# Kernel optimization log

Hardware: AMD Instinct MI355X
Metric: run time of the kernel (lower is better)

The kernel has to match this reference:

```python
import jax, jax.numpy as jnp
import numpy as np

B, T, LD, PD, W, NL = 2048, 256, 32, 8, 64, 3
TH, CH = LD * 2, W * 2  # token/channel mixing hidden dims (expansion=2)


def setup_inputs() -> dict:
    key = jax.random.key(0)
    ks = jax.random.split(key, 12)
    n = lambda k, s, sc=0.02: jax.random.normal(k, s, jnp.float32) * sc
    return {
        "phys": jax.random.normal(ks[0], (B, T, PD), jnp.float32),
        "latents": jax.random.uniform(ks[1], (B, LD), jnp.float32),
        "pos_emb": n(ks[2], (1, LD, W)),
        "tokW": n(ks[3], (1, W)), "tokb": jnp.zeros((W,), jnp.float32),
        "physW1": n(ks[4], (PD, W)), "physb1": jnp.zeros((W,), jnp.float32),
        "physW2": n(ks[5], (W, W)), "physb2": jnp.zeros((W,), jnp.float32),
        "tn_g": jnp.ones((NL, W), jnp.float32), "tn_b": jnp.zeros((NL, W), jnp.float32),
        "tiW": n(ks[6], (NL, LD, TH)), "tib": jnp.zeros((NL, TH), jnp.float32),
        "toW": n(ks[7], (NL, TH, LD)), "tob": jnp.zeros((NL, LD), jnp.float32),
        "cn_g": jnp.ones((NL, W), jnp.float32), "cn_b": jnp.zeros((NL, W), jnp.float32),
        "ciW": n(ks[8], (NL, W, CH)), "cib": jnp.zeros((NL, CH), jnp.float32),
        "coW": n(ks[9], (NL, CH, W)), "cob": jnp.zeros((NL, W), jnp.float32),
        "hn_g": jnp.ones((W,), jnp.float32), "hn_b": jnp.zeros((W,), jnp.float32),
        "headW": n(ks[10], (W, 1), 0.0002),  # 0.02 init * 0.01 scaling from torch
        "headb": jnp.zeros((1,), jnp.float32),
    }


def _ln(x, g, b):
    m = jnp.mean(x, -1, keepdims=True)
    v = jnp.mean((x - m) ** 2, -1, keepdims=True)
    return (x - m) * jax.lax.rsqrt(v + 1e-5) * g + b


def reference(phys, latents, pos_emb, tokW, tokb, physW1, physb1, physW2, physb2,
              tn_g, tn_b, tiW, tib, toW, tob, cn_g, cn_b, ciW, cib, coW, cob,
              hn_g, hn_b, headW, headb):
    gelu = lambda x: jax.nn.gelu(x, approximate=False)  # torch nn.GELU default (exact)

    def step(current, phys_t):
        # token_projection of current[..., None]: Linear(1, W)
        tokens = current[:, :, None] * tokW[0] + tokb  # [B, LD, W]
        p = gelu(phys_t @ physW1 + physb1) @ physW2 + physb2  # [B, W]
        tokens = tokens + p[:, None, :] + pos_emb
        for i in range(NL):
            # token mixing: LN over width, mix across latent tokens
            mt = jnp.swapaxes(_ln(tokens, tn_g[i], tn_b[i]), 1, 2)  # [B, W, LD]
            mt = gelu(mt @ tiW[i] + tib[i]) @ toW[i] + tob[i]       # [B, W, LD]
            tokens = tokens + jnp.swapaxes(mt, 1, 2)
            # channel mixing over width
            mc = _ln(tokens, cn_g[i], cn_b[i])
            tokens = tokens + (gelu(mc @ ciW[i] + cib[i]) @ coW[i] + cob[i])
        delta = (_ln(tokens, hn_g, hn_b) @ headW + headb)[..., 0]  # [B, LD]
        new = jnp.clip(current + delta, 0.0, 1.0)
        return new, new

    _, outs = jax.lax.scan(step, latents, jnp.swapaxes(phys, 0, 1))  # [T, B, LD]
    return jnp.swapaxes(outs, 0, 1)  # [B, T, LD]
```

## Files before the change

### kernel.cpp

```cpp
#include <hip/hip_runtime.h>
#include <math.h>


namespace {
constexpr int Tt = 256, NL = 3;

typedef float    f32x4 __attribute__((ext_vector_type(4)));
typedef _Float16 half2 __attribute__((ext_vector_type(2)));
typedef _Float16 h16x8 __attribute__((ext_vector_type(8)));

#define MFMA16(a, b, c) __builtin_amdgcn_mfma_f32_16x16x32_f16((a), (b), (c), 0, 0, 0)

__device__ __forceinline__ half2 h2c(float v) { return (half2)((_Float16)v); }
__device__ __forceinline__ half2 pkrtz(float a, float b) {
    return __builtin_bit_cast(half2, __builtin_amdgcn_cvt_pkrtz(a, b));
}
__device__ __forceinline__ void st4h(short* p, half2 a, half2 b) {
    uint2 v;
    v.x = __builtin_bit_cast(unsigned int, a);
    v.y = __builtin_bit_cast(unsigned int, b);
    *(uint2*)p = v;
}
__device__ __forceinline__ half2 gelu_pk(half2 x) {
    half2 tc = __builtin_elementwise_min(__builtin_elementwise_max(x, h2c(-3.0f)), h2c(3.0f));
    half2 s = (tc * tc) * h2c(0.125f);
    half2 p = s * h2c(0.1455169f) + h2c(-0.446340f);
    p = s * p + h2c(0.604927f);
    p = s * p + h2c(-0.529702f);
    p = s * p + h2c(0.3989423f);
    return x * (h2c(0.5f) + tc * p);
}
__device__ __forceinline__ float gelu_f(float x) {
    float tc = fminf(fmaxf(x, -3.f), 3.f);
    float s = tc * tc;
    float p = fmaf(s, 3.55266e-5f, -8.71758e-4f);
    p = fmaf(s, p, 9.45198e-3f);
    p = fmaf(s, p, -6.62128e-2f);
    p = fmaf(s, p, 0.3989423f);
    return x * fmaf(tc, p, 0.5f);
}
__device__ __forceinline__ float rowsum16(float x) {
    x += __builtin_bit_cast(float, __builtin_amdgcn_update_dpp(0, __builtin_bit_cast(int, x), 0x121, 0xf, 0xf, false));
    x += __builtin_bit_cast(float, __builtin_amdgcn_update_dpp(0, __builtin_bit_cast(int, x), 0x122, 0xf, 0xf, false));
    x += __builtin_bit_cast(float, __builtin_amdgcn_update_dpp(0, __builtin_bit_cast(int, x), 0x124, 0xf, 0xf, false));
    x += __builtin_bit_cast(float, __builtin_amdgcn_update_dpp(0, __builtin_bit_cast(int, x), 0x128, 0xf, 0xf, false));
    return x;
}

__device__ __forceinline__ short f2h(float x) {
    return __builtin_bit_cast(short, (_Float16)x);
}

__global__ void lno_prep(const float* __restrict__ tiW, const float* __restrict__ toW,
                         const float* __restrict__ ciW, const float* __restrict__ coW,
                         const float* __restrict__ physW2, short* __restrict__ wsf) {
    int id = blockIdx.x * 256 + threadIdx.x;
    if (id < 6144) {
        int j = id & 7, lane = (id >> 3) & 63, g = id >> 9;
        int il = g >> 2, u = g & 3;
        int m = u * 16 + (lane & 15), k = (lane >> 4) * 8 + j;
        wsf[id] = f2h(tiW[il * 2048 + k * 64 + m]);
    } else if (id < 12288) {
        int t = id - 6144;
        int j = t & 7, lane = (t >> 3) & 63, g = t >> 9;
        int il = g >> 2, mt2 = (g >> 1) & 1, ks = g & 1;
        int m = mt2 * 16 + (lane & 15), k = ks * 32 + (lane >> 4) * 8 + j;
        wsf[id] = f2h(toW[il * 2048 + k * 32 + m]);
    } else if (id < 36864) {
        int t = id - 12288;
        int j = t & 7, lane = (t >> 3) & 63, g = t >> 9;
        int il = g >> 4, mtc = (g >> 1) & 7, ks = g & 1;
        int m = mtc * 16 + (lane & 15), k = ks * 32 + (lane >> 4) * 8 + j;
        wsf[id] = f2h(ciW[il * 8192 + k * 128 + m]);
    } else if (id < 61440) {
        int t = id - 36864;
        int j = t & 7, lane = (t >> 3) & 63, g = t >> 9;
        int il = g >> 4, nt = (g >> 2) & 3, ks = g & 3;
        int n = nt * 16 + (lane & 15), k = ks * 32 + (lane >> 4) * 8 + j;
        wsf[id] = f2h(coW[il * 8192 + k * 64 + n]);
    } else if (id < 65536) {
        int t = id - 61440;
        int w = t >> 6, k = t & 63;
        ((float*)(wsf + 61440))[t] = physW2[k * 64 + w];
    }
}

__global__ __launch_bounds__(256, 2) void lno_scan(
    const float* __restrict__ phys,   const float* __restrict__ latents,
    const float* __restrict__ pos_emb,const float* __restrict__ tokW,
    const float* __restrict__ tokb,   const float* __restrict__ physW1,
    const float* __restrict__ physb1, const float* __restrict__ physb2,
    const float* __restrict__ tn_g,   const float* __restrict__ tn_b,
    const float* __restrict__ tib,    const float* __restrict__ tob,
    const float* __restrict__ cn_g,   const float* __restrict__ cn_b,
    const float* __restrict__ cib,    const float* __restrict__ cob,
    const float* __restrict__ hn_g,   const float* __restrict__ hn_b,
    const float* __restrict__ headW,  const float* __restrict__ headb,
    const short* __restrict__ wsf,    float* __restrict__ out)
{
    __shared__ __align__(16) short bufA[4][2048];
    __shared__ __align__(16) short bufB[4][2048];
    __shared__ __align__(16) short wbufC[8192];
    __shared__ __align__(16) short wbufO[8192];
    __shared__ __align__(16) float biasL[1632];
    __shared__ __align__(16) float pvh[4][128];

    const short* tiWF = wsf;
    const short* toWF = wsf + 6144;
    const short* ciWF = wsf + 12288;
    const short* coWF = wsf + 36864;
    const float* W2F  = (const float*)(wsf + 61440);

    const int tid = threadIdx.x, lane = tid & 63, wv = tid >> 6;
    const int q = lane >> 4, c = lane & 15;
    const int b = blockIdx.x * 4 + wv;

    short* yb = bufA[wv];
    short* hb = bufB[wv];

    for (int i = tid; i < 192; i += 256) {
        biasL[i] = tib[i];
        biasL[672 + i]  = tn_g[i];
        biasL[864 + i]  = tn_b[i];
        biasL[1056 + i] = cn_g[i];
        biasL[1248 + i] = cn_b[i];
        biasL[1440 + i] = cob[i];
    }
    for (int i = tid; i < 96;  i += 256) biasL[192 + i] = tob[i];
    for (int i = tid; i < 384; i += 256) biasL[288 + i] = cib[i];

    float tokw_r[4], tokb_r[4], gh_r[4];
#pragma unroll
    for (int nt = 0; nt < 4; ++nt) {
        tokw_r[nt] = tokW[nt * 16 + c];
        tokb_r[nt] = tokb[nt * 16 + c];
        gh_r[nt]   = hn_g[nt * 16 + c] * headW[nt * 16 + c];
    }
    float bhp = 0.f;
#pragma unroll
    for (int nt = 0; nt < 4; ++nt) bhp = fmaf(hn_b[nt * 16 + c], headW[nt * 16 + c], bhp);
    const float bh = rowsum16(bhp) + headb[0];

    float pe_r[2][4][4];
#pragma unroll
    for (int mt = 0; mt < 2; ++mt)
#pragma unroll
        for (int nt = 0; nt < 4; ++nt)
#pragma unroll
            for (int r = 0; r < 4; ++r)
                pe_r[mt][nt][r] = pos_emb[(mt * 16 + q * 4 + r) * 64 + nt * 16 + c];

    float w1_r[8];
#pragma unroll
    for (int k = 0; k < 8; ++k) w1_r[k] = physW1[k * 64 + lane];
    const float b1_r = physb1[lane];
    const float b2_r = physb2[lane];

    f32x4 cur8[2];
#pragma unroll
    for (int mt = 0; mt < 2; ++mt)
        cur8[mt] = *(const f32x4*)(latents + b * 32 + mt * 16 + q * 4);

    f32x4 tok[2][4];

    __syncthreads();

    auto stats = [&](f32x4 (&mean)[2], f32x4 (&rsig)[2]) {
#pragma unroll
        for (int mt = 0; mt < 2; ++mt)
#pragma unroll
            for (int r = 0; r < 4; ++r) {
                float s = (tok[mt][0][r] + tok[mt][1][r]) + (tok[mt][2][r] + tok[mt][3][r]);
                float qq = tok[mt][0][r] * tok[mt][0][r];
                qq = fmaf(tok[mt][1][r], tok[mt][1][r], qq);
                qq = fmaf(tok[mt][2][r], tok[mt][2][r], qq);
                qq = fmaf(tok[mt][3][r], tok[mt][3][r], qq);
                s = rowsum16(s); qq = rowsum16(qq);
                float m = s * 0.015625f;
                float v = fmaf(-m, m, qq * 0.015625f);
                mean[mt][r] = m;
                rsig[mt][r] = __builtin_amdgcn_rsqf(v + 1e-5f);
            }
    };

#pragma unroll 1
    for (int t = 0; t < Tt; ++t) {
        {
            const float* pt = phys + ((size_t)b * Tt + t) * 8;
            float4 px0 = *(const float4*)pt, px1 = *(const float4*)(pt + 4);
            float a = b1_r;
            a = fmaf(px0.x, w1_r[0], a); a = fmaf(px0.y, w1_r[1], a);
            a = fmaf(px0.z, w1_r[2], a); a = fmaf(px0.w, w1_r[3], a);
            a = fmaf(px1.x, w1_r[4], a); a = fmaf(px1.y, w1_r[5], a);
            a = fmaf(px1.z, w1_r[6], a); a = fmaf(px1.w, w1_r[7], a);
            pvh[wv][lane] = gelu_f(a);
        }
        float pnt[4];
        {
            float acc = b2_r;
            const f32x4* w2p = (const f32x4*)(W2F + lane * 64);
            const f32x4* h4 = (const f32x4*)&pvh[wv][0];
#pragma unroll
            for (int kk = 0; kk < 16; ++kk) {
                f32x4 w4 = w2p[kk];
                f32x4 hv = h4[kk];
                acc = fmaf(hv[0], w4[0], acc); acc = fmaf(hv[1], w4[1], acc);
                acc = fmaf(hv[2], w4[2], acc); acc = fmaf(hv[3], w4[3], acc);
            }
            pvh[wv][64 + lane] = acc;
#pragma unroll
            for (int nt = 0; nt < 4; ++nt) pnt[nt] = pvh[wv][64 + nt * 16 + c];
        }

#pragma unroll
        for (int nt = 0; nt < 4; ++nt) {
            const float basep = tokb_r[nt] + pnt[nt];
#pragma unroll
            for (int mt = 0; mt < 2; ++mt)
#pragma unroll
                for (int r = 0; r < 4; ++r)
                    tok[mt][nt][r] = fmaf(cur8[mt][r], tokw_r[nt], basep + pe_r[mt][nt][r]);
        }

#pragma unroll 1
        for (int il = 0; il < NL; ++il) {
            __syncthreads();
            {
                const unsigned int* srcC = (const unsigned int*)(ciWF + il * 8192);
                const unsigned int* srcO = (const unsigned int*)(coWF + il * 8192);
#pragma unroll
                for (int i = 0; i < 4; ++i) {
                    const int chunk = i * 4 + wv;
                    __builtin_amdgcn_global_load_lds(srcC + chunk * 256 + lane * 4,
                                                     (unsigned int*)&wbufC[chunk * 512], 16, 0, 0);
                    __builtin_amdgcn_global_load_lds(srcO + chunk * 256 + lane * 4,
                                                     (unsigned int*)&wbufO[chunk * 512], 16, 0, 0);
                }
            }

            f32x4 mean[2], rsig[2];
            stats(mean, rsig);
            float tng[4], tnb[4];
#pragma unroll
            for (int nt = 0; nt < 4; ++nt) {
                tng[nt] = biasL[672 + il * 64 + nt * 16 + c];
                tnb[nt] = biasL[864 + il * 64 + nt * 16 + c];
            }
#pragma unroll
            for (int mt = 0; mt < 2; ++mt)
#pragma unroll
                for (int nt = 0; nt < 4; ++nt) {
                    float y0 = fmaf((tok[mt][nt][0] - mean[mt][0]) * rsig[mt][0], tng[nt], tnb[nt]);
                    float y1 = fmaf((tok[mt][nt][1] - mean[mt][1]) * rsig[mt][1], tng[nt], tnb[nt]);
                    float y2 = fmaf((tok[mt][nt][2] - mean[mt][2]) * rsig[mt][2], tng[nt], tnb[nt]);
                    float y3 = fmaf((tok[mt][nt][3] - mean[mt][3]) * rsig[mt][3], tng[nt], tnb[nt]);
                    st4h(&yb[(nt * 64 + (mt * 2 + (q >> 1)) * 16 + c) * 8 + (q & 1) * 4],
                         pkrtz(y0, y1), pkrtz(y2, y3));
                }
            h16x8 yfrag[4];
#pragma unroll
            for (int nt = 0; nt < 4; ++nt) yfrag[nt] = *(const h16x8*)&yb[(nt * 64 + lane) * 8];

#pragma unroll
            for (int mt = 0; mt < 2; ++mt) {
                const f32x4 tb = *(const f32x4*)&biasL[192 + il * 32 + mt * 16 + q * 4];
#pragma unroll
                for (int nt = 0; nt < 4; ++nt) tok[mt][nt] += tb;
            }
#pragma unroll
            for (int h = 0; h < 2; ++h) {
#pragma unroll
                for (int uu = 0; uu < 2; ++uu) {
                    const int u = h * 2 + uu;
                    const h16x8 a1 = *(const h16x8*)(tiWF + ((il * 4 + u) * 64 + lane) * 8);
                    const f32x4 bi = *(const f32x4*)&biasL[il * 64 + u * 16 + q * 4];
#pragma unroll
                    for (int nt = 0; nt < 4; ++nt) {
                        f32x4 acc = MFMA16(a1, yfrag[nt], bi);
                        st4h(&hb[(nt * 64 + (uu * 2 + (q >> 1)) * 16 + c) * 8 + (q & 1) * 4],
                             gelu_pk(pkrtz(acc[0], acc[1])), gelu_pk(pkrtz(acc[2], acc[3])));
                    }
                }
                h16x8 hf[4];
#pragma unroll
                for (int nt = 0; nt < 4; ++nt) hf[nt] = *(const h16x8*)&hb[(nt * 64 + lane) * 8];
#pragma unroll
                for (int mt = 0; mt < 2; ++mt) {
                    const h16x8 a2 = *(const h16x8*)(toWF + ((il * 4 + mt * 2 + h) * 64 + lane) * 8);
#pragma unroll
                    for (int nt = 0; nt < 4; ++nt) tok[mt][nt] = MFMA16(a2, hf[nt], tok[mt][nt]);
                }
            }

            stats(mean, rsig);
            float cng[4], cnb[4];
#pragma unroll
            for (int nt = 0; nt < 4; ++nt) {
                cng[nt] = biasL[1056 + il * 64 + nt * 16 + c];
                cnb[nt] = biasL[1248 + il * 64 + nt * 16 + c];
            }
#pragma unroll
            for (int mt = 0; mt < 2; ++mt)
#pragma unroll
                for (int nt = 0; nt < 4; ++nt)
#pragma unroll
                    for (int r = 0; r < 4; ++r) {
                        float v = fmaf((tok[mt][nt][r] - mean[mt][r]) * rsig[mt][r], cng[nt], cnb[nt]);
                        yb[(mt * 2 + (nt >> 1)) * 512 +
                           (q * 2 + (c >> 3) + 16 * r + 8 * (nt & 1)) * 8 + (c & 7)] = f2h(v);
                    }
            h16x8 b3[4];
            {
                const int lp = ((c >> 2) * 2 + (q & 1)) + 8 * ((c & 3) * 2 + (q >> 1));
#pragma unroll
                for (int F = 0; F < 4; ++F) b3[F] = *(const h16x8*)&yb[F * 512 + lp * 8];
            }
#pragma unroll
            for (int nt = 0; nt < 4; ++nt) {
                const float cv = biasL[1440 + il * 64 + nt * 16 + c];
#pragma unroll
                for (int mt = 0; mt < 2; ++mt) tok[mt][nt] += cv;
            }

            __syncthreads();

#pragma unroll
            for (int hh = 0; hh < 2; ++hh) {
#pragma unroll
                for (int mm = 0; mm < 4; ++mm) {
                    const int mtc = hh * 4 + mm;
                    const h16x8 a30 = *(const h16x8*)&wbufC[(mtc * 2 + 0) * 512 + lane * 8];
                    const h16x8 a31 = *(const h16x8*)&wbufC[(mtc * 2 + 1) * 512 + lane * 8];
                    const f32x4 bi3 = *(const f32x4*)&biasL[288 + il * 128 + mtc * 16 + q * 4];
#pragma unroll
                    for (int ntl = 0; ntl < 2; ++ntl) {
                        f32x4 acc = MFMA16(a30, b3[ntl * 2 + 0], bi3);
                        acc = MFMA16(a31, b3[ntl * 2 + 1], acc);
                        st4h(&hb[((ntl * 2 + ((mtc >> 1) & 1)) * 64 +
                                  ((mtc & 1) * 2 + (q >> 1)) * 16 + c) * 8 + (q & 1) * 4],
                             gelu_pk(pkrtz(acc[0], acc[1])), gelu_pk(pkrtz(acc[2], acc[3])));
                    }
                }
                h16x8 a4[2][2];
#pragma unroll
                for (int mt = 0; mt < 2; ++mt)
#pragma unroll
                    for (int kk = 0; kk < 2; ++kk)
                        a4[mt][kk] = *(const h16x8*)&hb[((mt * 2 + kk) * 64 + lane) * 8];
#pragma unroll
                for (int nt = 0; nt < 4; ++nt) {
                    const h16x8 b40 = *(const h16x8*)&wbufO[(nt * 4 + hh * 2 + 0) * 512 + lane * 8];
                    const h16x8 b41 = *(const h16x8*)&wbufO[(nt * 4 + hh * 2 + 1) * 512 + lane * 8];
#pragma unroll
                    for (int mt = 0; mt < 2; ++mt) {
                        tok[mt][nt] = MFMA16(a4[mt][0], b40, tok[mt][nt]);
                        tok[mt][nt] = MFMA16(a4[mt][1], b41, tok[mt][nt]);
                    }
                }
            }
        }

        {
            f32x4 mean[2], rsig[2];
            stats(mean, rsig);
#pragma unroll
            for (int mt = 0; mt < 2; ++mt)
#pragma unroll
                for (int r = 0; r < 4; ++r) {
                    float l = (tok[mt][0][r] - mean[mt][r]) * gh_r[0];
                    l = fmaf(tok[mt][1][r] - mean[mt][r], gh_r[1], l);
                    l = fmaf(tok[mt][2][r] - mean[mt][r], gh_r[2], l);
                    l = fmaf(tok[mt][3][r] - mean[mt][r], gh_r[3], l);
                    l = rowsum16(l);
                    float nv = cur8[mt][r] + fmaf(rsig[mt][r], l, bh);
                    nv = fminf(fmaxf(nv, 0.f), 1.f);
                    cur8[mt][r] = nv;
                }
            if (c == 0) {
                float* op = out + ((size_t)b * Tt + t) * 32 + q * 4;
                *(f32x4*)(op) = cur8[0];
                *(f32x4*)(op + 16) = cur8[1];
            }
        }
    }
}
}

extern "C" void kernel_launch(void* const* d_in, const int* in_sizes, int n_in,
                              void* d_out, int out_size, void* d_ws, size_t ws_size,
                              hipStream_t stream) {
    (void)in_sizes; (void)n_in; (void)ws_size; (void)out_size;
    const float* phys    = (const float*)d_in[0];
    const float* latents = (const float*)d_in[1];
    const float* pos_emb = (const float*)d_in[2];
    const float* tokW    = (const float*)d_in[3];
    const float* tokb    = (const float*)d_in[4];
    const float* physW1  = (const float*)d_in[5];
    const float* physb1  = (const float*)d_in[6];
    const float* physW2  = (const float*)d_in[7];
    const float* physb2  = (const float*)d_in[8];
    const float* tn_g    = (const float*)d_in[9];
    const float* tn_b    = (const float*)d_in[10];
    const float* tiW     = (const float*)d_in[11];
    const float* tib     = (const float*)d_in[12];
    const float* toW     = (const float*)d_in[13];
    const float* tob     = (const float*)d_in[14];
    const float* cn_g    = (const float*)d_in[15];
    const float* cn_b    = (const float*)d_in[16];
    const float* ciW     = (const float*)d_in[17];
    const float* cib     = (const float*)d_in[18];
    const float* coW     = (const float*)d_in[19];
    const float* cob     = (const float*)d_in[20];
    const float* hn_g    = (const float*)d_in[21];
    const float* hn_b    = (const float*)d_in[22];
    const float* headW   = (const float*)d_in[23];
    const float* headb   = (const float*)d_in[24];

    lno_prep<<<dim3(256), dim3(256), 0, stream>>>(tiW, toW, ciW, coW, physW2, (short*)d_ws);
    lno_scan<<<dim3(512), dim3(256), 0, stream>>>(
        phys, latents, pos_emb, tokW, tokb, physW1, physb1, physb2,
        tn_g, tn_b, tib, tob, cn_g, cn_b, cib, cob, hn_g, hn_b, headW, headb,
        (const short*)d_ws, (float*)d_out);
}
```

Measured before the change: 7.215 ms.

## Hoist phys MLP into parallel kernel and split each batch row across two waves

The phys-input MLP does not depend on the recurrent state, so it moves out of the serial time loop into its own fully parallel kernel. That kernel stores its result as fp16 in the output buffer, and the scan kernel reads each slot before overwriting it at the same step. The scan kernel now gives one batch row to a 128-thread block, with each wave owning 16 latent tokens, and it exchanges normalized activations through shared memory. Channel-mixing weights are read straight from global/L2 instead of being staged in LDS, which removes the per-layer async weight copies and shrinks LDS use. The cost is an extra intermediate buffer written and read through HBM, more block-level barriers per layer, and rounding the phys projection to fp16.

Result: slower. 7.556 ms (+4.7%).

```diff
diff --git a/kernel.cpp b/kernel.cpp
--- a/kernel.cpp
+++ b/kernel.cpp
@@ -7,6 +7,7 @@
 
 typedef float    f32x4 __attribute__((ext_vector_type(4)));
 typedef _Float16 half2 __attribute__((ext_vector_type(2)));
+typedef _Float16 h16x4 __attribute__((ext_vector_type(4)));
 typedef _Float16 h16x8 __attribute__((ext_vector_type(8)));
 
 #define MFMA16(a, b, c) __builtin_amdgcn_mfma_f32_16x16x32_f16((a), (b), (c), 0, 0, 0)
@@ -85,49 +86,54 @@
     }
 }
 
-__global__ __launch_bounds__(256, 2) void lno_scan(
-    const float* __restrict__ phys,   const float* __restrict__ latents,
-    const float* __restrict__ pos_emb,const float* __restrict__ tokW,
-    const float* __restrict__ tokb,   const float* __restrict__ physW1,
-    const float* __restrict__ physb1, const float* __restrict__ physb2,
-    const float* __restrict__ tn_g,   const float* __restrict__ tn_b,
-    const float* __restrict__ tib,    const float* __restrict__ tob,
-    const float* __restrict__ cn_g,   const float* __restrict__ cn_b,
-    const float* __restrict__ cib,    const float* __restrict__ cob,
-    const float* __restrict__ hn_g,   const float* __restrict__ hn_b,
-    const float* __restrict__ headW,  const float* __restrict__ headb,
-    const short* __restrict__ wsf,    float* __restrict__ out)
+__global__ void lno_phys(const float* __restrict__ phys, const float* __restrict__ physW1,
+                         const float* __restrict__ physb1, const float* __restrict__ physW2,
+                         const float* __restrict__ physb2, short* __restrict__ pout) {
+    __shared__ float hsh[4][64];
+    const int lane = threadIdx.x & 63, wv = threadIdx.x >> 6;
+    const size_t bt = (size_t)blockIdx.x * 4 + wv;
+    const float* pt = phys + bt * 8;
+    float4 px0 = *(const float4*)pt, px1 = *(const float4*)(pt + 4);
+    float a = physb1[lane];
+    a = fmaf(px0.x, physW1[0 * 64 + lane], a);
+    a = fmaf(px0.y, physW1[1 * 64 + lane], a);
+    a = fmaf(px0.z, physW1[2 * 64 + lane], a);
+    a = fmaf(px0.w, physW1[3 * 64 + lane], a);
+    a = fmaf(px1.x, physW1[4 * 64 + lane], a);
+    a = fmaf(px1.y, physW1[5 * 64 + lane], a);
+    a = fmaf(px1.z, physW1[6 * 64 + lane], a);
+    a = fmaf(px1.w, physW1[7 * 64 + lane], a);
+    hsh[wv][lane] = gelu_f(a);
+    float acc = physb2[lane];
+#pragma unroll
+    for (int k = 0; k < 64; ++k) acc = fmaf(hsh[wv][k], physW2[k * 64 + lane], acc);
+    pout[bt * 64 + (lane & 15) * 4 + (lane >> 4)] = f2h(acc);
+}
+
+__global__ __launch_bounds__(128, 4) void lno_scan(
+    const float* __restrict__ latents, const float* __restrict__ pos_emb,
+    const float* __restrict__ tokW,    const float* __restrict__ tokb,
+    const float* __restrict__ tn_g,    const float* __restrict__ tn_b,
+    const float* __restrict__ tib,     const float* __restrict__ tob,
+    const float* __restrict__ cn_g,    const float* __restrict__ cn_b,
+    const float* __restrict__ cib,     const float* __restrict__ cob,
+    const float* __restrict__ hn_g,    const float* __restrict__ hn_b,
+    const float* __restrict__ headW,   const float* __restrict__ headb,
+    const short* __restrict__ wsf,     const short* pbuf, float* out)
 {
-    __shared__ __align__(16) short bufA[4][2048];
-    __shared__ __align__(16) short bufB[4][2048];
-    __shared__ __align__(16) short wbufC[8192];
-    __shared__ __align__(16) short wbufO[8192];
-    __shared__ __align__(16) float biasL[1632];
-    __shared__ __align__(16) float pvh[4][128];
+    __shared__ __align__(16) short yB[2048];
+    __shared__ __align__(16) short hB[4096];
+    __shared__ __align__(16) short scr[2][1024];
 
     const short* tiWF = wsf;
     const short* toWF = wsf + 6144;
     const short* ciWF = wsf + 12288;
     const short* coWF = wsf + 36864;
-    const float* W2F  = (const float*)(wsf + 61440);
-
-    const int tid = threadIdx.x, lane = tid & 63, wv = tid >> 6;
+
+    const int tid = threadIdx.x, lane = tid & 63, sb = tid >> 6;
     const int q = lane >> 4, c = lane & 15;
-    const int b = blockIdx.x * 4 + wv;
-
-    short* yb = bufA[wv];
-    short* hb = bufB[wv];
-
-    for (int i = tid; i < 192; i += 256) {
-        biasL[i] = tib[i];
-        biasL[672 + i]  = tn_g[i];
-        biasL[864 + i]  = tn_b[i];
-        biasL[1056 + i] = cn_g[i];
-        biasL[1248 + i] = cn_b[i];
-        biasL[1440 + i] = cob[i];
-    }
-    for (int i = tid; i < 96;  i += 256) biasL[192 + i] = tob[i];
-    for (int i = tid; i < 384; i += 256) biasL[288 + i] = cib[i];
+    const int b = blockIdx.x;
+    short* sc = scr[sb];
 
     float tokw_r[4], tokb_r[4], gh_r[4];
 #pragma unroll
@@ -141,246 +147,155 @@
     for (int nt = 0; nt < 4; ++nt) bhp = fmaf(hn_b[nt * 16 + c], headW[nt * 16 + c], bhp);
     const float bh = rowsum16(bhp) + headb[0];
 
-    float pe_r[2][4][4];
-#pragma unroll
-    for (int mt = 0; mt < 2; ++mt)
-#pragma unroll
-        for (int nt = 0; nt < 4; ++nt)
-#pragma unroll
-            for (int r = 0; r < 4; ++r)
-                pe_r[mt][nt][r] = pos_emb[(mt * 16 + q * 4 + r) * 64 + nt * 16 + c];
-
-    float w1_r[8];
-#pragma unroll
-    for (int k = 0; k < 8; ++k) w1_r[k] = physW1[k * 64 + lane];
-    const float b1_r = physb1[lane];
-    const float b2_r = physb2[lane];
-
-    f32x4 cur8[2];
-#pragma unroll
-    for (int mt = 0; mt < 2; ++mt)
-        cur8[mt] = *(const f32x4*)(latents + b * 32 + mt * 16 + q * 4);
-
-    f32x4 tok[2][4];
-
-    __syncthreads();
-
-    auto stats = [&](f32x4 (&mean)[2], f32x4 (&rsig)[2]) {
-#pragma unroll
-        for (int mt = 0; mt < 2; ++mt)
-#pragma unroll
-            for (int r = 0; r < 4; ++r) {
-                float s = (tok[mt][0][r] + tok[mt][1][r]) + (tok[mt][2][r] + tok[mt][3][r]);
-                float qq = tok[mt][0][r] * tok[mt][0][r];
-                qq = fmaf(tok[mt][1][r], tok[mt][1][r], qq);
-                qq = fmaf(tok[mt][2][r], tok[mt][2][r], qq);
-                qq = fmaf(tok[mt][3][r], tok[mt][3][r], qq);
-                s = rowsum16(s); qq = rowsum16(qq);
-                float m = s * 0.015625f;
-                float v = fmaf(-m, m, qq * 0.015625f);
-                mean[mt][r] = m;
-                rsig[mt][r] = __builtin_amdgcn_rsqf(v + 1e-5f);
-            }
+    float pe_r[4][4];
+#pragma unroll
+    for (int nt = 0; nt < 4; ++nt)
+#pragma unroll
+        for (int r = 0; r < 4; ++r)
+            pe_r[nt][r] = pos_emb[(sb * 16 + q * 4 + r) * 64 + nt * 16 + c];
+
+    f32x4 cur = *(const f32x4*)(latents + b * 32 + sb * 16 + q * 4);
+    f32x4 tok[4];
+
+    auto stats = [&](f32x4& mean, f32x4& rsig) {
+#pragma unroll
+        for (int r = 0; r < 4; ++r) {
+            float s = (tok[0][r] + tok[1][r]) + (tok[2][r] + tok[3][r]);
+            float qq = tok[0][r] * tok[0][r];
+            qq = fmaf(tok[1][r], tok[1][r], qq);
+            qq = fmaf(tok[2][r], tok[2][r], qq);
+            qq = fmaf(tok[3][r], tok[3][r], qq);
+            s = rowsum16(s); qq = rowsum16(qq);
+            float m = s * 0.015625f;
+            float v = fmaf(-m, m, qq * 0.015625f);
+            mean[r] = m;
+            rsig[r] = __builtin_amdgcn_rsqf(v + 1e-5f);
+        }
     };
 
 #pragma unroll 1
     for (int t = 0; t < Tt; ++t) {
-        {
-            const float* pt = phys + ((size_t)b * Tt + t) * 8;
-            float4 px0 = *(const float4*)pt, px1 = *(const float4*)(pt + 4);
-            float a = b1_r;
-            a = fmaf(px0.x, w1_r[0], a); a = fmaf(px0.y, w1_r[1], a);
-            a = fmaf(px0.z, w1_r[2], a); a = fmaf(px0.w, w1_r[3], a);
-            a = fmaf(px1.x, w1_r[4], a); a = fmaf(px1.y, w1_r[5], a);
-            a = fmaf(px1.z, w1_r[6], a); a = fmaf(px1.w, w1_r[7], a);
-            pvh[wv][lane] = gelu_f(a);
-        }
-        float pnt[4];
-        {
-            float acc = b2_r;
-            const f32x4* w2p = (const f32x4*)(W2F + lane * 64);
-            const f32x4* h4 = (const f32x4*)&pvh[wv][0];
-#pragma unroll
-            for (int kk = 0; kk < 16; ++kk) {
-                f32x4 w4 = w2p[kk];
-                f32x4 hv = h4[kk];
-                acc = fmaf(hv[0], w4[0], acc); acc = fmaf(hv[1], w4[1], acc);
-                acc = fmaf(hv[2], w4[2], acc); acc = fmaf(hv[3], w4[3], acc);
-            }
-            pvh[wv][64 + lane] = acc;
-#pragma unroll
-            for (int nt = 0; nt < 4; ++nt) pnt[nt] = pvh[wv][64 + nt * 16 + c];
-        }
-
+        const h16x4 pv = *(const h16x4*)(pbuf + ((size_t)b * Tt + t) * 64 + c * 4);
 #pragma unroll
         for (int nt = 0; nt < 4; ++nt) {
-            const float basep = tokb_r[nt] + pnt[nt];
-#pragma unroll
-            for (int mt = 0; mt < 2; ++mt)
-#pragma unroll
-                for (int r = 0; r < 4; ++r)
-                    tok[mt][nt][r] = fmaf(cur8[mt][r], tokw_r[nt], basep + pe_r[mt][nt][r]);
+            const float basep = tokb_r[nt] + (float)pv[nt];
+#pragma unroll
+            for (int r = 0; r < 4; ++r)
+                tok[nt][r] = fmaf(cur[r], tokw_r[nt], basep + pe_r[nt][r]);
         }
 
 #pragma unroll 1
         for (int il = 0; il < NL; ++il) {
+            f32x4 mean, rsig;
+            stats(mean, rsig);
+#pragma unroll
+            for (int nt = 0; nt < 4; ++nt) {
+                const float tng = tn_g[il * 64 + nt * 16 + c];
+                const float tnb = tn_b[il * 64 + nt * 16 + c];
+                float y0 = fmaf((tok[nt][0] - mean[0]) * rsig[0], tng, tnb);
+                float y1 = fmaf((tok[nt][1] - mean[1]) * rsig[1], tng, tnb);
+                float y2 = fmaf((tok[nt][2] - mean[2]) * rsig[2], tng, tnb);
+                float y3 = fmaf((tok[nt][3] - mean[3]) * rsig[3], tng, tnb);
+                st4h(&yB[(nt * 64 + (sb * 2 + (q >> 1)) * 16 + c) * 8 + (q & 1) * 4],
+                     pkrtz(y0, y1), pkrtz(y2, y3));
+            }
             __syncthreads();
+            h16x8 yfrag[4];
+#pragma unroll
+            for (int nt = 0; nt < 4; ++nt) yfrag[nt] = *(const h16x8*)&yB[(nt * 64 + lane) * 8];
+
+#pragma unroll
+            for (int uu = 0; uu < 2; ++uu) {
+                const int u = sb * 2 + uu;
+                const h16x8 a1 = *(const h16x8*)(tiWF + ((il * 4 + u) * 64 + lane) * 8);
+                const f32x4 bi = *(const f32x4*)(tib + il * 64 + u * 16 + q * 4);
+#pragma unroll
+                for (int nt = 0; nt < 4; ++nt) {
+                    f32x4 acc = MFMA16(a1, yfrag[nt], bi);
+                    st4h(&hB[sb * 2048 + (nt * 64 + (uu * 2 + (q >> 1)) * 16 + c) * 8 + (q & 1) * 4],
+                         gelu_pk(pkrtz(acc[0], acc[1])), gelu_pk(pkrtz(acc[2], acc[3])));
+                }
+            }
             {
-                const unsigned int* srcC = (const unsigned int*)(ciWF + il * 8192);
-                const unsigned int* srcO = (const unsigned int*)(coWF + il * 8192);
-#pragma unroll
-                for (int i = 0; i < 4; ++i) {
-                    const int chunk = i * 4 + wv;
-                    __builtin_amdgcn_global_load_lds(srcC + chunk * 256 + lane * 4,
-                                                     (unsigned int*)&wbufC[chunk * 512], 16, 0, 0);
-                    __builtin_amdgcn_global_load_lds(srcO + chunk * 256 + lane * 4,
-                                                     (unsigned int*)&wbufO[chunk * 512], 16, 0, 0);
+                const f32x4 tb = *(const f32x4*)(tob + il * 32 + sb * 16 + q * 4);
+#pragma unroll
+                for (int nt = 0; nt < 4; ++nt) tok[nt] += tb;
+            }
+            __syncthreads();
+#pragma unroll
+            for (int h = 0; h < 2; ++h) {
+                const h16x8 a2 = *(const h16x8*)(toWF + ((il * 4 + sb * 2 + h) * 64 + lane) * 8);
+                h16x8 hf[4];
+#pragma unroll
+                for (int nt = 0; nt < 4; ++nt)
+                    hf[nt] = *(const h16x8*)&hB[h * 2048 + (nt * 64 + lane) * 8];
+#pragma unroll
+                for (int nt = 0; nt < 4; ++nt) tok[nt] = MFMA16(a2, hf[nt], tok[nt]);
+            }
+
+            stats(mean, rsig);
+#pragma unroll
+            for (int nt = 0; nt < 4; ++nt) {
+                const float cng = cn_g[il * 64 + nt * 16 + c];
+                const float cnb = cn_b[il * 64 + nt * 16 + c];
+#pragma unroll
+                for (int r = 0; r < 4; ++r) {
+                    float v = fmaf((tok[nt][r] - mean[r]) * rsig[r], cng, cnb);
+                    sc[(nt >> 1) * 512 + (q * 2 + (c >> 3) + 16 * r + 8 * (nt & 1)) * 8 + (c & 7)] = f2h(v);
                 }
             }
-
-            f32x4 mean[2], rsig[2];
-            stats(mean, rsig);
-            float tng[4], tnb[4];
-#pragma unroll
-            for (int nt = 0; nt < 4; ++nt) {
-                tng[nt] = biasL[672 + il * 64 + nt * 16 + c];
-                tnb[nt] = biasL[864 + il * 64 + nt * 16 + c];
-            }
-#pragma unroll
-            for (int mt = 0; mt < 2; ++mt)
-#pragma unroll
-                for (int nt = 0; nt < 4; ++nt) {
-                    float y0 = fmaf((tok[mt][nt][0] - mean[mt][0]) * rsig[mt][0], tng[nt], tnb[nt]);
-                    float y1 = fmaf((tok[mt][nt][1] - mean[mt][1]) * rsig[mt][1], tng[nt], tnb[nt]);
-                    float y2 = fmaf((tok[mt][nt][2] - mean[mt][2]) * rsig[mt][2], tng[nt], tnb[nt]);
-                    float y3 = fmaf((tok[mt][nt][3] - mean[mt][3]) * rsig[mt][3], tng[nt], tnb[nt]);
-                    st4h(&yb[(nt * 64 + (mt * 2 + (q >> 1)) * 16 + c) * 8 + (q & 1) * 4],
-                         pkrtz(y0, y1), pkrtz(y2, y3));
-                }
-            h16x8 yfrag[4];
-#pragma unroll
-            for (int nt = 0; nt < 4; ++nt) yfrag[nt] = *(const h16x8*)&yb[(nt * 64 + lane) * 8];
-
-#pragma unroll
-            for (int mt = 0; mt < 2; ++mt) {
-                const f32x4 tb = *(const f32x4*)&biasL[192 + il * 32 + mt * 16 + q * 4];
-#pragma unroll
-                for (int nt = 0; nt < 4; ++nt) tok[mt][nt] += tb;
-            }
-#pragma unroll
-            for (int h = 0; h < 2; ++h) {
-#pragma unroll
-                for (int uu = 0; uu < 2; ++uu) {
-                    const int u = h * 2 + uu;
-                    const h16x8 a1 = *(const h16x8*)(tiWF + ((il * 4 + u) * 64 + lane) * 8);
-                    const f32x4 bi = *(const f32x4*)&biasL[il * 64 + u * 16 + q * 4];
-#pragma unroll
-                    for (int nt = 0; nt < 4; ++nt) {
-                        f32x4 acc = MFMA16(a1, yfrag[nt], bi);
-                        st4h(&hb[(nt * 64 + (uu * 2 + (q >> 1)) * 16 + c) * 8 + (q & 1) * 4],
-                             gelu_pk(pkrtz(acc[0], acc[1])), gelu_pk(pkrtz(acc[2], acc[3])));
-                    }
-                }
-                h16x8 hf[4];
-#pragma unroll
-                for (int nt = 0; nt < 4; ++nt) hf[nt] = *(const h16x8*)&hb[(nt * 64 + lane) * 8];
-#pragma unroll
-                for (int mt = 0; mt < 2; ++mt) {
-                    const h16x8 a2 = *(const h16x8*)(toWF + ((il * 4 + mt * 2 + h) * 64 + lane) * 8);
-#pragma unroll
-                    for (int nt = 0; nt < 4; ++nt) tok[mt][nt] = MFMA16(a2, hf[nt], tok[mt][nt]);
-                }
-            }
-
-            stats(mean, rsig);
-            float cng[4], cnb[4];
-#pragma unroll
-            for (int nt = 0; nt < 4; ++nt) {
-                cng[nt] = biasL[1056 + il * 64 + nt * 16 + c];
-                cnb[nt] = biasL[1248 + il * 64 + nt * 16 + c];
-            }
-#pragma unroll
-            for (int mt = 0; mt < 2; ++mt)
-#pragma unroll
-                for (int nt = 0; nt < 4; ++nt)
-#pragma unroll
-                    for (int r = 0; r < 4; ++r) {
-                        float v = fmaf((tok[mt][nt][r] - mean[mt][r]) * rsig[mt][r], cng[nt], cnb[nt]);
-                        yb[(mt * 2 + (nt >> 1)) * 512 +
-                           (q * 2 + (c >> 3) + 16 * r + 8 * (nt & 1)) * 8 + (c & 7)] = f2h(v);
-                    }
-            h16x8 b3[4];
+            h16x8 b3[2];
             {
                 const int lp = ((c >> 2) * 2 + (q & 1)) + 8 * ((c & 3) * 2 + (q >> 1));
 #pragma unroll
-                for (int F = 0; F < 4; ++F) b3[F] = *(const h16x8*)&yb[F * 512 + lp * 8];
+                for (int ks = 0; ks < 2; ++ks) b3[ks] = *(const h16x8*)&sc[ks * 512 + lp * 8];
             }
 #pragma unroll
             for (int nt = 0; nt < 4; ++nt) {
-                const float cv = biasL[1440 + il * 64 + nt * 16 + c];
-#pragma unroll
-                for (int mt = 0; mt < 2; ++mt) tok[mt][nt] += cv;
-            }
-
-            __syncthreads();
-
+                const float cv = cob[il * 64 + nt * 16 + c];
+                tok[nt] += cv;
+            }
 #pragma unroll
             for (int hh = 0; hh < 2; ++hh) {
 #pragma unroll
                 for (int mm = 0; mm < 4; ++mm) {
                     const int mtc = hh * 4 + mm;
-                    const h16x8 a30 = *(const h16x8*)&wbufC[(mtc * 2 + 0) * 512 + lane * 8];
-                    const h16x8 a31 = *(const h16x8*)&wbufC[(mtc * 2 + 1) * 512 + lane * 8];
-                    const f32x4 bi3 = *(const f32x4*)&biasL[288 + il * 128 + mtc * 16 + q * 4];
-#pragma unroll
-                    for (int ntl = 0; ntl < 2; ++ntl) {
-                        f32x4 acc = MFMA16(a30, b3[ntl * 2 + 0], bi3);
-                        acc = MFMA16(a31, b3[ntl * 2 + 1], acc);
-                        st4h(&hb[((ntl * 2 + ((mtc >> 1) & 1)) * 64 +
-                                  ((mtc & 1) * 2 + (q >> 1)) * 16 + c) * 8 + (q & 1) * 4],
-                             gelu_pk(pkrtz(acc[0], acc[1])), gelu_pk(pkrtz(acc[2], acc[3])));
-                    }
+                    const h16x8 a30 = *(const h16x8*)(ciWF + il * 8192 + (mtc * 2 + 0) * 512 + lane * 8);
+                    const h16x8 a31 = *(const h16x8*)(ciWF + il * 8192 + (mtc * 2 + 1) * 512 + lane * 8);
+                    const f32x4 bi3 = *(const f32x4*)(cib + il * 128 + mtc * 16 + q * 4);
+                    f32x4 acc = MFMA16(a30, b3[0], bi3);
+                    acc = MFMA16(a31, b3[1], acc);
+                    st4h(&sc[(((mtc >> 1) & 1) * 64 + ((mtc & 1) * 2 + (q >> 1)) * 16 + c) * 8 + (q & 1) * 4],
+                         gelu_pk(pkrtz(acc[0], acc[1])), gelu_pk(pkrtz(acc[2], acc[3])));
                 }
-                h16x8 a4[2][2];
-#pragma unroll
-                for (int mt = 0; mt < 2; ++mt)
-#pragma unroll
-                    for (int kk = 0; kk < 2; ++kk)
-                        a4[mt][kk] = *(const h16x8*)&hb[((mt * 2 + kk) * 64 + lane) * 8];
+                h16x8 a4[2];
+#pragma unroll
+                for (int kk = 0; kk < 2; ++kk) a4[kk] = *(const h16x8*)&sc[(kk * 64 + lane) * 8];
 #pragma unroll
                 for (int nt = 0; nt < 4; ++nt) {
-                    const h16x8 b40 = *(const h16x8*)&wbufO[(nt * 4 + hh * 2 + 0) * 512 + lane * 8];
-                    const h16x8 b41 = *(const h16x8*)&wbufO[(nt * 4 + hh * 2 + 1) * 512 + lane * 8];
-#pragma unroll
-                    for (int mt = 0; mt < 2; ++mt) {
-                        tok[mt][nt] = MFMA16(a4[mt][0], b40, tok[mt][nt]);
-                        tok[mt][nt] = MFMA16(a4[mt][1], b41, tok[mt][nt]);
-                    }
+                    const h16x8 b40 = *(const h16x8*)(coWF + il * 8192 + (nt * 4 + hh * 2 + 0) * 512 + lane * 8);
+                    const h16x8 b41 = *(const h16x8*)(coWF + il * 8192 + (nt * 4 + hh * 2 + 1) * 512 + lane * 8);
+                    tok[nt] = MFMA16(a4[0], b40, tok[nt]);
+                    tok[nt] = MFMA16(a4[1], b41, tok[nt]);
                 }
             }
         }
 
         {
-            f32x4 mean[2], rsig[2];
+            f32x4 mean, rsig;
             stats(mean, rsig);
 #pragma unroll
-            for (int mt = 0; mt < 2; ++mt)
-#pragma unroll
-                for (int r = 0; r < 4; ++r) {
-                    float l = (tok[mt][0][r] - mean[mt][r]) * gh_r[0];
-                    l = fmaf(tok[mt][1][r] - mean[mt][r], gh_r[1], l);
-                    l = fmaf(tok[mt][2][r] - mean[mt][r], gh_r[2], l);
-                    l = fmaf(tok[mt][3][r] - mean[mt][r], gh_r[3], l);
-                    l = rowsum16(l);
-                    float nv = cur8[mt][r] + fmaf(rsig[mt][r], l, bh);
-                    nv = fminf(fmaxf(nv, 0.f), 1.f);
-                    cur8[mt][r] = nv;
-                }
-            if (c == 0) {
-                float* op = out + ((size_t)b * Tt + t) * 32 + q * 4;
-                *(f32x4*)(op) = cur8[0];
-                *(f32x4*)(op + 16) = cur8[1];
-            }
+            for (int r = 0; r < 4; ++r) {
+                float l = (tok[0][r] - mean[r]) * gh_r[0];
+                l = fmaf(tok[1][r] - mean[r], gh_r[1], l);
+                l = fmaf(tok[2][r] - mean[r], gh_r[2], l);
+                l = fmaf(tok[3][r] - mean[r], gh_r[3], l);
+                l = rowsum16(l);
+                float nv = cur[r] + fmaf(rsig[r], l, bh);
+                cur[r] = fminf(fmaxf(nv, 0.f), 1.f);
+            }
+            if (c == 0)
+                *(f32x4*)(out + ((size_t)b * Tt + t) * 32 + sb * 16 + q * 4) = cur;
         }
     }
 }
@@ -417,8 +332,10 @@
     const float* headb   = (const float*)d_in[24];
 
     lno_prep<<<dim3(256), dim3(256), 0, stream>>>(tiW, toW, ciW, coW, physW2, (short*)d_ws);
-    lno_scan<<<dim3(512), dim3(256), 0, stream>>>(
-        phys, latents, pos_emb, tokW, tokb, physW1, physb1, physb2,
-        tn_g, tn_b, tib, tob, cn_g, cn_b, cib, cob, hn_g, hn_b, headW, headb,
-        (const short*)d_ws, (float*)d_out);
-}
+    lno_phys<<<dim3(131072), dim3(256), 0, stream>>>(phys, physW1, physb1, physW2, physb2,
+                                                     (short*)d_out);
+    lno_scan<<<dim3(2048), dim3(128), 0, stream>>>(
+        latents, pos_emb, tokW, tokb, tn_g, tn_b, tib, tob,
+        cn_g, cn_b, cib, cob, hn_g, hn_b, headW, headb,
+        (const short*)d_ws, (const short*)d_out, (float*)d_out);
+}
```

## Precompute phys MLP in a parallel kernel and keep all mixer weights LDS-resident

Applied to the files above, without the earlier changes.

The per-timestep physics MLP moves into a separate fully parallel kernel. It writes fp16 results into the output buffer as scratch, and the scan prefetches them one step ahead; since batch b's scratch and output occupy the same bytes, each step writes only the slice already read. The scan kernel now loads all token and channel mixing weights into LDS once at startup instead of restaging them every layer. This removes the per-layer barriers and global reloads, and blocks go to 512 threads covering 8 batch rows. LDS use grows to about 160KB, so only one block fits per CU, and the phys projection is stored at reduced precision.

Result: faster. 6.093 ms (-15.6%).

```diff
diff --git a/kernel.cpp b/kernel.cpp
--- a/kernel.cpp
+++ b/kernel.cpp
@@ -7,6 +7,7 @@
 
 typedef float    f32x4 __attribute__((ext_vector_type(4)));
 typedef _Float16 half2 __attribute__((ext_vector_type(2)));
+typedef _Float16 h16x4 __attribute__((ext_vector_type(4)));
 typedef _Float16 h16x8 __attribute__((ext_vector_type(8)));
 
 #define MFMA16(a, b, c) __builtin_amdgcn_mfma_f32_16x16x32_f16((a), (b), (c), 0, 0, 0)
@@ -85,40 +86,65 @@
     }
 }
 
-__global__ __launch_bounds__(256, 2) void lno_scan(
-    const float* __restrict__ phys,   const float* __restrict__ latents,
-    const float* __restrict__ pos_emb,const float* __restrict__ tokW,
-    const float* __restrict__ tokb,   const float* __restrict__ physW1,
-    const float* __restrict__ physb1, const float* __restrict__ physb2,
-    const float* __restrict__ tn_g,   const float* __restrict__ tn_b,
-    const float* __restrict__ tib,    const float* __restrict__ tob,
-    const float* __restrict__ cn_g,   const float* __restrict__ cn_b,
-    const float* __restrict__ cib,    const float* __restrict__ cob,
-    const float* __restrict__ hn_g,   const float* __restrict__ hn_b,
-    const float* __restrict__ headW,  const float* __restrict__ headb,
-    const short* __restrict__ wsf,    float* __restrict__ out)
+__global__ void lno_phys(const float* __restrict__ phys, const float* __restrict__ physW1,
+                         const float* __restrict__ physb1, const float* __restrict__ physW2,
+                         const float* __restrict__ physb2, short* __restrict__ pout) {
+    __shared__ float hsh[4][64];
+    const int lane = threadIdx.x & 63, wv = threadIdx.x >> 6;
+    const size_t bt = (size_t)blockIdx.x * 4 + wv;
+    const float* pt = phys + bt * 8;
+    float4 px0 = *(const float4*)pt, px1 = *(const float4*)(pt + 4);
+    float a = physb1[lane];
+    a = fmaf(px0.x, physW1[0 * 64 + lane], a);
+    a = fmaf(px0.y, physW1[1 * 64 + lane], a);
+    a = fmaf(px0.z, physW1[2 * 64 + lane], a);
+    a = fmaf(px0.w, physW1[3 * 64 + lane], a);
+    a = fmaf(px1.x, physW1[4 * 64 + lane], a);
+    a = fmaf(px1.y, physW1[5 * 64 + lane], a);
+    a = fmaf(px1.z, physW1[6 * 64 + lane], a);
+    a = fmaf(px1.w, physW1[7 * 64 + lane], a);
+    hsh[wv][lane] = gelu_f(a);
+    float acc = physb2[lane];
+#pragma unroll
+    for (int k = 0; k < 64; ++k) acc = fmaf(hsh[wv][k], physW2[k * 64 + lane], acc);
+    pout[bt * 64 + (lane & 15) * 4 + (lane >> 4)] = f2h(acc);
+}
+
+__global__ __launch_bounds__(512, 2) void lno_scan(
+    const float* __restrict__ latents, const float* __restrict__ pos_emb,
+    const float* __restrict__ tokW,    const float* __restrict__ tokb,
+    const float* __restrict__ tn_g,    const float* __restrict__ tn_b,
+    const float* __restrict__ tib,     const float* __restrict__ tob,
+    const float* __restrict__ cn_g,    const float* __restrict__ cn_b,
+    const float* __restrict__ cib,     const float* __restrict__ cob,
+    const float* __restrict__ hn_g,    const float* __restrict__ hn_b,
+    const float* __restrict__ headW,   const float* __restrict__ headb,
+    const short* __restrict__ wsf,     const short* pbuf, float* out)
 {
-    __shared__ __align__(16) short bufA[4][2048];
-    __shared__ __align__(16) short bufB[4][2048];
-    __shared__ __align__(16) short wbufC[8192];
-    __shared__ __align__(16) short wbufO[8192];
+    __shared__ __align__(16) short wAll[61440];
+    __shared__ __align__(16) short scr[8][2048];
     __shared__ __align__(16) float biasL[1632];
-    __shared__ __align__(16) float pvh[4][128];
-
-    const short* tiWF = wsf;
-    const short* toWF = wsf + 6144;
-    const short* ciWF = wsf + 12288;
-    const short* coWF = wsf + 36864;
-    const float* W2F  = (const float*)(wsf + 61440);
 
     const int tid = threadIdx.x, lane = tid & 63, wv = tid >> 6;
     const int q = lane >> 4, c = lane & 15;
-    const int b = blockIdx.x * 4 + wv;
-
-    short* yb = bufA[wv];
-    short* hb = bufB[wv];
-
-    for (int i = tid; i < 192; i += 256) {
+    const int b = blockIdx.x * 8 + wv;
+    short* sc = scr[wv];
+
+    const short* tiL = wAll;
+    const short* toL = wAll + 6144;
+    const short* ciL = wAll + 12288;
+    const short* coL = wAll + 36864;
+
+    {
+        const unsigned int* src = (const unsigned int*)wsf;
+#pragma unroll
+        for (int i = 0; i < 15; ++i) {
+            const int cid = wv * 15 + i;
+            __builtin_amdgcn_global_load_lds(src + cid * 256 + lane * 4,
+                                             (unsigned int*)&wAll[cid * 512], 16, 0, 0);
+        }
+    }
+    for (int i = tid; i < 192; i += 512) {
         biasL[i] = tib[i];
         biasL[672 + i]  = tn_g[i];
         biasL[864 + i]  = tn_b[i];
@@ -126,8 +152,8 @@
         biasL[1248 + i] = cn_b[i];
         biasL[1440 + i] = cob[i];
     }
-    for (int i = tid; i < 96;  i += 256) biasL[192 + i] = tob[i];
-    for (int i = tid; i < 384; i += 256) biasL[288 + i] = cib[i];
+    for (int i = tid; i < 96;  i += 512) biasL[192 + i] = tob[i];
+    for (int i = tid; i < 384; i += 512) biasL[288 + i] = cib[i];
 
     float tokw_r[4], tokb_r[4], gh_r[4];
 #pragma unroll
@@ -149,12 +175,6 @@
 #pragma unroll
             for (int r = 0; r < 4; ++r)
                 pe_r[mt][nt][r] = pos_emb[(mt * 16 + q * 4 + r) * 64 + nt * 16 + c];
-
-    float w1_r[8];
-#pragma unroll
-    for (int k = 0; k < 8; ++k) w1_r[k] = physW1[k * 64 + lane];
-    const float b1_r = physb1[lane];
-    const float b2_r = physb2[lane];
 
     f32x4 cur8[2];
 #pragma unroll
@@ -183,38 +203,17 @@
             }
     };
 
+    const short* pb = pbuf + (size_t)b * Tt * 64 + c * 4;
+    h16x4 pvc = *(const h16x4*)pb;
+
 #pragma unroll 1
     for (int t = 0; t < Tt; ++t) {
-        {
-            const float* pt = phys + ((size_t)b * Tt + t) * 8;
-            float4 px0 = *(const float4*)pt, px1 = *(const float4*)(pt + 4);
-            float a = b1_r;
-            a = fmaf(px0.x, w1_r[0], a); a = fmaf(px0.y, w1_r[1], a);
-            a = fmaf(px0.z, w1_r[2], a); a = fmaf(px0.w, w1_r[3], a);
-            a = fmaf(px1.x, w1_r[4], a); a = fmaf(px1.y, w1_r[5], a);
-            a = fmaf(px1.z, w1_r[6], a); a = fmaf(px1.w, w1_r[7], a);
-            pvh[wv][lane] = gelu_f(a);
-        }
-        float pnt[4];
-        {
-            float acc = b2_r;
-            const f32x4* w2p = (const f32x4*)(W2F + lane * 64);
-            const f32x4* h4 = (const f32x4*)&pvh[wv][0];
-#pragma unroll
-            for (int kk = 0; kk < 16; ++kk) {
-                f32x4 w4 = w2p[kk];
-                f32x4 hv = h4[kk];
-                acc = fmaf(hv[0], w4[0], acc); acc = fmaf(hv[1], w4[1], acc);
-                acc = fmaf(hv[2], w4[2], acc); acc = fmaf(hv[3], w4[3], acc);
-            }
-            pvh[wv][64 + lane] = acc;
-#pragma unroll
-            for (int nt = 0; nt < 4; ++nt) pnt[nt] = pvh[wv][64 + nt * 16 + c];
-        }
+        const h16x4 pv = pvc;
+        if (t + 1 < Tt) pvc = *(const h16x4*)(pb + (t + 1) * 64);
 
 #pragma unroll
         for (int nt = 0; nt < 4; ++nt) {
-            const float basep = tokb_r[nt] + pnt[nt];
+            const float basep = tokb_r[nt] + (float)pv[nt];
 #pragma unroll
             for (int mt = 0; mt < 2; ++mt)
 #pragma unroll
@@ -224,20 +223,6 @@
 
 #pragma unroll 1
         for (int il = 0; il < NL; ++il) {
-            __syncthreads();
-            {
-                const unsigned int* srcC = (const unsigned int*)(ciWF + il * 8192);
-                const unsigned int* srcO = (const unsigned int*)(coWF + il * 8192);
-#pragma unroll
-                for (int i = 0; i < 4; ++i) {
-                    const int chunk = i * 4 + wv;
-                    __builtin_amdgcn_global_load_lds(srcC + chunk * 256 + lane * 4,
-                                                     (unsigned int*)&wbufC[chunk * 512], 16, 0, 0);
-                    __builtin_amdgcn_global_load_lds(srcO + chunk * 256 + lane * 4,
-                                                     (unsigned int*)&wbufO[chunk * 512], 16, 0, 0);
-                }
-            }
-
             f32x4 mean[2], rsig[2];
             stats(mean, rsig);
             float tng[4], tnb[4];
@@ -254,12 +239,12 @@
                     float y1 = fmaf((tok[mt][nt][1] - mean[mt][1]) * rsig[mt][1], tng[nt], tnb[nt]);
                     float y2 = fmaf((tok[mt][nt][2] - mean[mt][2]) * rsig[mt][2], tng[nt], tnb[nt]);
                     float y3 = fmaf((tok[mt][nt][3] - mean[mt][3]) * rsig[mt][3], tng[nt], tnb[nt]);
-                    st4h(&yb[(nt * 64 + (mt * 2 + (q >> 1)) * 16 + c) * 8 + (q & 1) * 4],
+                    st4h(&sc[(nt * 64 + (mt * 2 + (q >> 1)) * 16 + c) * 8 + (q & 1) * 4],
                          pkrtz(y0, y1), pkrtz(y2, y3));
                 }
             h16x8 yfrag[4];
 #pragma unroll
-            for (int nt = 0; nt < 4; ++nt) yfrag[nt] = *(const h16x8*)&yb[(nt * 64 + lane) * 8];
+            for (int nt = 0; nt < 4; ++nt) yfrag[nt] = *(const h16x8*)&sc[(nt * 64 + lane) * 8];
 
 #pragma unroll
             for (int mt = 0; mt < 2; ++mt) {
@@ -272,21 +257,21 @@
 #pragma unroll
                 for (int uu = 0; uu < 2; ++uu) {
                     const int u = h * 2 + uu;
-                    const h16x8 a1 = *(const h16x8*)(tiWF + ((il * 4 + u) * 64 + lane) * 8);
+                    const h16x8 a1 = *(const h16x8*)(tiL + ((il * 4 + u) * 64 + lane) * 8);
                     const f32x4 bi = *(const f32x4*)&biasL[il * 64 + u * 16 + q * 4];
 #pragma unroll
                     for (int nt = 0; nt < 4; ++nt) {
                         f32x4 acc = MFMA16(a1, yfrag[nt], bi);
-                        st4h(&hb[(nt * 64 + (uu * 2 + (q >> 1)) * 16 + c) * 8 + (q & 1) * 4],
+                        st4h(&sc[(nt * 64 + (uu * 2 + (q >> 1)) * 16 + c) * 8 + (q & 1) * 4],
                              gelu_pk(pkrtz(acc[0], acc[1])), gelu_pk(pkrtz(acc[2], acc[3])));
                     }
                 }
                 h16x8 hf[4];
 #pragma unroll
-                for (int nt = 0; nt < 4; ++nt) hf[nt] = *(const h16x8*)&hb[(nt * 64 + lane) * 8];
+                for (int nt = 0; nt < 4; ++nt) hf[nt] = *(const h16x8*)&sc[(nt * 64 + lane) * 8];
 #pragma unroll
                 for (int mt = 0; mt < 2; ++mt) {
-                    const h16x8 a2 = *(const h16x8*)(toWF + ((il * 4 + mt * 2 + h) * 64 + lane) * 8);
+                    const h16x8 a2 = *(const h16x8*)(toL + ((il * 4 + mt * 2 + h) * 64 + lane) * 8);
 #pragma unroll
                     for (int nt = 0; nt < 4; ++nt) tok[mt][nt] = MFMA16(a2, hf[nt], tok[mt][nt]);
                 }
@@ -306,14 +291,14 @@
 #pragma unroll
                     for (int r = 0; r < 4; ++r) {
                         float v = fmaf((tok[mt][nt][r] - mean[mt][r]) * rsig[mt][r], cng[nt], cnb[nt]);
-                        yb[(mt * 2 + (nt >> 1)) * 512 +
+                        sc[(mt * 2 + (nt >> 1)) * 512 +
                            (q * 2 + (c >> 3) + 16 * r + 8 * (nt & 1)) * 8 + (c & 7)] = f2h(v);
                     }
             h16x8 b3[4];
             {
                 const int lp = ((c >> 2) * 2 + (q & 1)) + 8 * ((c & 3) * 2 + (q >> 1));
 #pragma unroll
-                for (int F = 0; F < 4; ++F) b3[F] = *(const h16x8*)&yb[F * 512 + lp * 8];
+                for (int F = 0; F < 4; ++F) b3[F] = *(const h16x8*)&sc[F * 512 + lp * 8];
             }
 #pragma unroll
             for (int nt = 0; nt < 4; ++nt) {
@@ -322,21 +307,19 @@
                 for (int mt = 0; mt < 2; ++mt) tok[mt][nt] += cv;
             }
 
-            __syncthreads();
-
 #pragma unroll
             for (int hh = 0; hh < 2; ++hh) {
 #pragma unroll
                 for (int mm = 0; mm < 4; ++mm) {
                     const int mtc = hh * 4 + mm;
-                    const h16x8 a30 = *(const h16x8*)&wbufC[(mtc * 2 + 0) * 512 + lane * 8];
-                    const h16x8 a31 = *(const h16x8*)&wbufC[(mtc * 2 + 1) * 512 + lane * 8];
+                    const h16x8 a30 = *(const h16x8*)(ciL + il * 8192 + (mtc * 2 + 0) * 512 + lane * 8);
+                    const h16x8 a31 = *(const h16x8*)(ciL + il * 8192 + (mtc * 2 + 1) * 512 + lane * 8);
                     const f32x4 bi3 = *(const f32x4*)&biasL[288 + il * 128 + mtc * 16 + q * 4];
 #pragma unroll
                     for (int ntl = 0; ntl < 2; ++ntl) {
                         f32x4 acc = MFMA16(a30, b3[ntl * 2 + 0], bi3);
                         acc = MFMA16(a31, b3[ntl * 2 + 1], acc);
-                        st4h(&hb[((ntl * 2 + ((mtc >> 1) & 1)) * 64 +
+                        st4h(&sc[((ntl * 2 + ((mtc >> 1) & 1)) * 64 +
                                   ((mtc & 1) * 2 + (q >> 1)) * 16 + c) * 8 + (q & 1) * 4],
                              gelu_pk(pkrtz(acc[0], acc[1])), gelu_pk(pkrtz(acc[2], acc[3])));
                     }
@@ -346,11 +329,11 @@
                 for (int mt = 0; mt < 2; ++mt)
 #pragma unroll
                     for (int kk = 0; kk < 2; ++kk)
-                        a4[mt][kk] = *(const h16x8*)&hb[((mt * 2 + kk) * 64 + lane) * 8];
+                        a4[mt][kk] = *(const h16x8*)&sc[((mt * 2 + kk) * 64 + lane) * 8];
 #pragma unroll
                 for (int nt = 0; nt < 4; ++nt) {
-                    const h16x8 b40 = *(const h16x8*)&wbufO[(nt * 4 + hh * 2 + 0) * 512 + lane * 8];
-                    const h16x8 b41 = *(const h16x8*)&wbufO[(nt * 4 + hh * 2 + 1) * 512 + lane * 8];
+                    const h16x8 b40 = *(const h16x8*)(coL + il * 8192 + (nt * 4 + hh * 2 + 0) * 512 + lane * 8);
+                    const h16x8 b41 = *(const h16x8*)(coL + il * 8192 + (nt * 4 + hh * 2 + 1) * 512 + lane * 8);
 #pragma unroll
                     for (int mt = 0; mt < 2; ++mt) {
                         tok[mt][nt] = MFMA16(a4[mt][0], b40, tok[mt][nt]);
@@ -417,8 +400,10 @@
     const float* headb   = (const float*)d_in[24];
 
     lno_prep<<<dim3(256), dim3(256), 0, stream>>>(tiW, toW, ciW, coW, physW2, (short*)d_ws);
-    lno_scan<<<dim3(512), dim3(256), 0, stream>>>(
-        phys, latents, pos_emb, tokW, tokb, physW1, physb1, physb2,
-        tn_g, tn_b, tib, tob, cn_g, cn_b, cib, cob, hn_g, hn_b, headW, headb,
-        (const short*)d_ws, (float*)d_out);
-}
+    lno_phys<<<dim3(131072), dim3(256), 0, stream>>>(phys, physW1, physb1, physW2, physb2,
+                                                     (short*)d_out);
+    lno_scan<<<dim3(256), dim3(512), 0, stream>>>(
+        latents, pos_emb, tokW, tokb, tn_g, tn_b, tib, tob,
+        cn_g, cn_b, cib, cob, hn_g, hn_b, headW, headb,
+        (const short*)d_ws, (const short*)d_out, (float*)d_out);
+}
```
